# Kernel tuning notes

Hardware: AMD Instinct MI355X
Metric: run time of the kernel (lower is better)

The kernel has to match this reference:

```python
import jax, jax.numpy as jnp
import numpy as np

MEM_SIZE = 2000
FEA_DIM = 256
FMAP = 32
BATCH = 32
SHRINK = 0.0025
EPS = 1e-12


def setup_inputs() -> dict:
    key = jax.random.key(0)
    k1, k2, k3, k4 = jax.random.split(key, 4)
    stdv = 1.0 / np.sqrt(FEA_DIM)
    inp = {
        "input": jax.random.normal(k1, (BATCH, FEA_DIM, FMAP, FMAP), dtype=jnp.float32),
        "label_batch": jax.random.randint(k2, (BATCH,), 0, 2),
        "weight": jax.random.uniform(k3, (MEM_SIZE, FEA_DIM), dtype=jnp.float32, minval=-stdv, maxval=stdv),
        "pos_embedding": jax.random.normal(k4, (1, FEA_DIM, FMAP, FMAP), dtype=jnp.float32),
    }
    return inp


def _forward(x, weight, pos_embedding):
    b, c, h, w = x.shape
    m = weight.shape[0]
    x = x + pos_embedding  # pos=True
    xr = x.transpose(0, 2, 3, 1).reshape(-1, c)  # [b*h*w, c]
    # addressing: linear -> softmax over memory slots
    att = jax.nn.softmax(jnp.einsum('nc,mc->nm', xr, weight), axis=1)  # [N, m]
    # compact loss: MSE to nearest memory item (argmax of att before shrink)
    idx = jnp.argmax(att, axis=1)
    pos_item = weight[idx]  # [N, c]
    compact_loss = jnp.mean((xr - pos_item) ** 2)
    # distance loss: hinge on pairwise squared distances between memory items
    sq = jnp.sum(weight * weight, axis=1)
    d2 = sq[:, None] + sq[None, :] - 2.0 * (weight @ weight.T)  # [m, m]
    dist = 1.0 - d2
    dist = dist * (dist > 0).astype(dist.dtype)
    dist = jnp.triu(dist, k=1)
    distance_loss = dist.sum() * 2.0 / (m * (m - 1))
    # hard shrink relu + L1 normalize (shrink_thres > 0)
    att = jax.nn.relu(att - SHRINK) * att / (jnp.abs(att - SHRINK) + EPS)
    att = att / jnp.maximum(jnp.sum(jnp.abs(att), axis=1, keepdims=True), EPS)
    # memory read
    out = jnp.einsum('nm,mc->nc', att, weight)
    out = out.reshape(b, h, w, c).transpose(0, 3, 1, 2)
    return out, compact_loss, distance_loss


def reference(input, label_batch, weight, pos_embedding):
    return _forward(input, weight, pos_embedding)
```

## Files before the change

kernel.cpp:

```cpp
#include <hip/hip_runtime.h>
#include <hip/hip_bf16.h>

typedef unsigned char u8;
typedef unsigned short u16;
typedef unsigned int u32;
typedef long long s64;
typedef float f32x4 __attribute__((ext_vector_type(4)));
typedef long long s64x2 __attribute__((ext_vector_type(2)));

#define MEM    2000
#define FEA    256
#define SLSTR  2064
#define OSTR   265
#define XRS    264
#define POOLSZ 66048
#define OUTN   8388608

__device__ __forceinline__ u32 f2e4m3(float x) {
    float ax = fabsf(x);
    u32 s = (__builtin_bit_cast(u32, x) >> 24) & 0x80u;
    if (ax >= 448.f) return s | 0x7e;
    if (ax < 0.015625f) {
        int q = (int)rintf(ax * 512.f);
        return s | (u32)q;
    }
    int e = (int)(__builtin_bit_cast(u32, ax) >> 23) - 127;
    float scale = __builtin_bit_cast(float, (u32)((127 - e + 3) << 23));
    int q = (int)rintf(ax * scale);
    int E = e + 7;
    if (q == 16) { q = 8; E += 1; if (E > 15) return s | 0x7e; }
    return s | (u32)(E << 3) | (u32)(q & 7);
}
__device__ __forceinline__ u32 f2e4m3_fast(float v) {
    u32 u = __builtin_bit_cast(u32, v);
    u += 0x0007FFFFu + ((u >> 20) & 1u);
    int bb = (int)(u >> 20) - 0x3C0;
    return bb < 0 ? 0u : (u32)bb;
}

__global__ __launch_bounds__(256) void prep_kernel(const float* __restrict__ W,
                                                   u8* __restrict__ WTc,
                                                   u8* __restrict__ Wc,
                                                   float* __restrict__ sqv,
                                                   float* __restrict__ loss) {
    const int blk = blockIdx.x, t = threadIdx.x;
    const int m0 = blk * 8;
    {
        const int sl = t >> 5, cl = t & 31;
        const int slot = m0 + sl;
        const int ch0 = cl * 8;
        const float* wr = W + slot * 256 + ch0;
        f32x4 v0 = *(const f32x4*)wr;
        f32x4 v1 = *(const f32x4*)(wr + 4);
        float ss = v0[0]*v0[0] + v0[1]*v0[1] + v0[2]*v0[2] + v0[3]*v0[3]
                 + v1[0]*v1[0] + v1[1]*v1[1] + v1[2]*v1[2] + v1[3]*v1[3];
        ss += __shfl_xor(ss, 1); ss += __shfl_xor(ss, 2); ss += __shfl_xor(ss, 4);
        ss += __shfl_xor(ss, 8); ss += __shfl_xor(ss, 16);
        if (cl == 0) sqv[slot] = ss;
        const int c = slot >> 6, s = slot & 63;
        const int kk = cl >> 2, agp = cl & 3;
        const int kp = kk >> 1, klo = kk & 1;
        u32 lo = 0, hi = 0;
#pragma unroll
        for (int i = 0; i < 4; ++i) {
            lo |= f2e4m3(v0[i] * 16.f) << (i * 8);
            hi |= f2e4m3(v1[i] * 16.f) << (i * 8);
        }
        u8* dst = Wc + c * 16384 + (size_t)((kp * 4 + agp) * 64 + s) * 16 + klo * 8;
        *(u32*)dst = lo;
        *(u32*)(dst + 4) = hi;
    }
    {
        const int ch = t;
        const int chunk = m0 >> 6;
        const int kl0 = m0 & 63;
        const int klo = kl0 >> 5, agp = (kl0 & 31) >> 3;
        u32 lo = 0, hi = 0;
#pragma unroll
        for (int i = 0; i < 8; ++i) {
            u32 bb = f2e4m3(W[(m0 + i) * 256 + ch] * 16.f);
            if (i < 4) lo |= bb << (i * 8); else hi |= bb << ((i - 4) * 8);
        }
        u8* dst = WTc + chunk * 16384 + ch * 64 + agp * 16 + klo * 8;
        *(u32*)dst = lo;
        *(u32*)(dst + 4) = hi;
    }
    if (blk == 0 && t == 0) {
        loss[0] = 0.0f;
        loss[1] = -2000.0f / (2000.0f * 1999.0f);
    }
}

__global__ __launch_bounds__(512, 1) void main_kernel(
        const float* __restrict__ inp, const float* __restrict__ posb,
        const u8* __restrict__ Wc, const u8* __restrict__ WTc,
        const float* __restrict__ sqv, float* __restrict__ out,
        float* __restrict__ loss) {
    __shared__ __align__(16) u8 pool[POOLSZ];
    __shared__ float sPM[4][32];
    __shared__ int   sPI[4][32];
    __shared__ float sPZ[4][32];
    __shared__ float sPD[4][32];
    __shared__ float sSS[8][32];
    __shared__ float sMax[32];
    __shared__ float sThr[32];
    __shared__ float sInv[32];

    const int t = threadIdx.x;
    const int w = t >> 6, lane = t & 63;
    const int ar = lane & 15, ag = lane >> 4;
    const int blk = blockIdx.x, b = blk >> 5, hw0 = (blk & 31) << 5;
    const int prot = ((blk >> 3) & 15) * 2;
    const int q = w & 3, rt = w >> 2;
    const int row_a = rt * 16 + ar;

    {
        const int hw = t & 31, cg = t >> 5;
        const float* ip = inp + (size_t)b * 262144 + hw0 + hw;
        const float* pp = posb + hw0 + hw;
        float ss = 0.f;
        u8* xrow = pool + hw * XRS + cg * 16;
#pragma unroll
        for (int j = 0; j < 8; ++j) {
            const int ch = cg * 16 + 2 * j;
            float v0 = ip[ch * 1024] + pp[ch * 1024];
            float v1 = ip[(ch + 1) * 1024] + pp[(ch + 1) * 1024];
            ss += v0 * v0 + v1 * v1;
            u16 pk2 = (u16)(f2e4m3(v0 * 4.f) | (f2e4m3(v1 * 4.f) << 8));
            *(u16*)(xrow + 2 * j) = pk2;
        }
        ss += __shfl_xor(ss, 32);
        if (lane < 32) sSS[w][lane] = ss;
    }
    __syncthreads();

    s64 xB[8];
#pragma unroll
    for (int kk = 0; kk < 8; ++kk)
        xB[kk] = *(const s64*)(pool + row_a * XRS + kk * 32 + ag * 8);

    f32x4 acc[32];
    const int c31 = (31 - prot) & 31;
    {
        const u8* wbase = Wc + ag * 1024 + (q * 16 + ar) * 16;
#pragma unroll
        for (int c = 0; c < 32; ++c) {
            const int pc = (c + prot) & 31;
            const u8* p = wbase + pc * 16384;
            s64x2 w0 = *(const s64x2*)(p);
            s64x2 w1 = *(const s64x2*)(p + 4096);
            s64x2 w2 = *(const s64x2*)(p + 8192);
            s64x2 w3 = *(const s64x2*)(p + 12288);
            f32x4 a = {0.f, 0.f, 0.f, 0.f};
            a = __builtin_amdgcn_mfma_f32_16x16x32_fp8_fp8(w0[0], xB[0], a, 0, 0, 0);
            a = __builtin_amdgcn_mfma_f32_16x16x32_fp8_fp8(w0[1], xB[1], a, 0, 0, 0);
            a = __builtin_amdgcn_mfma_f32_16x16x32_fp8_fp8(w1[0], xB[2], a, 0, 0, 0);
            a = __builtin_amdgcn_mfma_f32_16x16x32_fp8_fp8(w1[1], xB[3], a, 0, 0, 0);
            a = __builtin_amdgcn_mfma_f32_16x16x32_fp8_fp8(w2[0], xB[4], a, 0, 0, 0);
            a = __builtin_amdgcn_mfma_f32_16x16x32_fp8_fp8(w2[1], xB[5], a, 0, 0, 0);
            a = __builtin_amdgcn_mfma_f32_16x16x32_fp8_fp8(w3[0], xB[6], a, 0, 0, 0);
            a = __builtin_amdgcn_mfma_f32_16x16x32_fp8_fp8(w3[1], xB[7], a, 0, 0, 0);
            if (c == c31 && q != 0) { a[0] = -3e38f; a[1] = -3e38f; a[2] = -3e38f; a[3] = -3e38f; }
            acc[c] = a;
        }
    }

    {
        float bm = -3e38f; int bi = 0x7fffffff;
#pragma unroll
        for (int c = 0; c < 32; ++c) {
            const int cb = (((c + prot) & 31) << 6) + q * 16 + ag * 4;
#pragma unroll
            for (int e = 0; e < 4; ++e) {
                float f = acc[c][e];
                int id = cb + e;
                if (f > bm || (f == bm && id < bi)) { bm = f; bi = id; }
            }
        }
#pragma unroll
        for (int d = 16; d < 64; d <<= 1) {
            float om = __shfl_xor(bm, d);
            int   oi = __shfl_xor(bi, d);
            if (om > bm || (om == bm && oi < bi)) { bm = om; bi = oi; }
        }
        if (lane < 16) { sPM[q][rt * 16 + lane] = bm; sPI[q][rt * 16 + lane] = bi; }
    }
    __syncthreads();

    if (t < 32) {
        float mx = sPM[0][t]; int bid = sPI[0][t];
#pragma unroll
        for (int qq = 1; qq < 4; ++qq) {
            float m2 = sPM[qq][t]; int i2 = sPI[qq][t];
            if (m2 > mx || (m2 == mx && i2 < bid)) { mx = m2; bid = i2; }
        }
        sMax[t] = mx;
        float ssq = 0.f;
#pragma unroll
        for (int ww = 0; ww < 8; ++ww) ssq += sSS[ww][t];
        float term = ssq - 2.f * (mx * 0.015625f) + sqv[bid];
#pragma unroll
        for (int d = 1; d < 32; d <<= 1) term += __shfl_xor(term, d);
        if (t == 0) atomicAdd(loss, term * (1.0f / 8388608.0f));
    }
    __syncthreads();

    {
        const float mxv = sMax[row_a];
        float z = 0.f;
#pragma unroll
        for (int c = 0; c < 32; ++c)
#pragma unroll
            for (int e = 0; e < 4; ++e) {
                float a_ = __expf((acc[c][e] - mxv) * 0.015625f);
                acc[c][e] = a_;
                z += a_;
            }
        z += __shfl_xor(z, 16); z += __shfl_xor(z, 32);
        if (lane < 16) sPZ[q][rt * 16 + lane] = z;
    }
    __syncthreads();
    if (t < 32) sThr[t] = 0.0025f * (sPZ[0][t] + sPZ[1][t] + sPZ[2][t] + sPZ[3][t]);
    __syncthreads();

    {
        const float thrv = sThr[row_a];
        const int newoff = (((q * 2 + (ag >> 1)) & 3) << 4) | ((q >> 1) << 3) | ((ag & 1) << 2);
        const int rowbase = row_a * SLSTR + newoff;
        float den = 0.f;
#pragma unroll
        for (int c = 0; c < 32; ++c) {
            const int off = rowbase + (((c + prot) & 31) << 6);
            u32 pk = 0;
#pragma unroll
            for (int e = 0; e < 4; ++e) {
                float a_ = acc[c][e];
                if (a_ > thrv) { den += a_; pk |= f2e4m3_fast(a_ * 64.f) << (e * 8); }
            }
            *(u32*)(pool + off) = pk;
        }
        den += __shfl_xor(den, 16); den += __shfl_xor(den, 32);
        if (lane < 16) sPD[q][rt * 16 + lane] = den;
    }
    __syncthreads();
    if (t < 32) {
        float dd = sPD[0][t] + sPD[1][t] + sPD[2][t] + sPD[3][t];
        sInv[t] = dd > 0.f ? 1.0f / (1024.0f * dd) : 0.0f;
    }
    __syncthreads();

    const int ch0 = (w * 2) * 16 + ar;
    const int ch1 = ch0 + 16;
    const u8* sLr0 = pool + ar * SLSTR + ag * 16;
    const u8* sLr1 = pool + (16 + ar) * SLSTR + ag * 16;
    const u8* wt0 = WTc + ch0 * 64 + ag * 16;
    const u8* wt1 = WTc + ch1 * 64 + ag * 16;
    f32x4 o00 = {0.f,0.f,0.f,0.f}, o01 = {0.f,0.f,0.f,0.f};
    f32x4 o10 = {0.f,0.f,0.f,0.f}, o11 = {0.f,0.f,0.f,0.f};
#pragma unroll
    for (int c = 0; c < 32; ++c) {
        const int pc = (c + prot) & 31;
        const int cc64 = pc << 6;
        s64x2 B0 = *(const s64x2*)(wt0 + pc * 16384);
        s64x2 B1 = *(const s64x2*)(wt1 + pc * 16384);
        s64x2 A0 = *(const s64x2*)(sLr0 + cc64);
        s64x2 A1 = *(const s64x2*)(sLr1 + cc64);
        o00 = __builtin_amdgcn_mfma_f32_16x16x32_fp8_fp8(A0[0], B0[0], o00, 0, 0, 0);
        o00 = __builtin_amdgcn_mfma_f32_16x16x32_fp8_fp8(A0[1], B0[1], o00, 0, 0, 0);
        o01 = __builtin_amdgcn_mfma_f32_16x16x32_fp8_fp8(A1[0], B0[0], o01, 0, 0, 0);
        o01 = __builtin_amdgcn_mfma_f32_16x16x32_fp8_fp8(A1[1], B0[1], o01, 0, 0, 0);
        o10 = __builtin_amdgcn_mfma_f32_16x16x32_fp8_fp8(A0[0], B1[0], o10, 0, 0, 0);
        o10 = __builtin_amdgcn_mfma_f32_16x16x32_fp8_fp8(A0[1], B1[1], o10, 0, 0, 0);
        o11 = __builtin_amdgcn_mfma_f32_16x16x32_fp8_fp8(A1[0], B1[0], o11, 0, 0, 0);
        o11 = __builtin_amdgcn_mfma_f32_16x16x32_fp8_fp8(A1[1], B1[1], o11, 0, 0, 0);
    }
    __syncthreads();

    {
        float* sO = (float*)pool;
#pragma unroll
        for (int i = 0; i < 4; ++i) {
            int r0 = ag * 4 + i, r1 = 16 + ag * 4 + i;
            sO[r0 * OSTR + ch0] = o00[i] * sInv[r0];
            sO[r1 * OSTR + ch0] = o01[i] * sInv[r1];
            sO[r0 * OSTR + ch1] = o10[i] * sInv[r0];
            sO[r1 * OSTR + ch1] = o11[i] * sInv[r1];
        }
    }
    __syncthreads();
    {
        const float* sO = (const float*)pool;
        const int hw = t & 31, cq = t >> 5;
        float* op = out + (size_t)b * 262144 + hw0 + hw;
#pragma unroll
        for (int i = 0; i < 16; ++i) {
            int ch = cq + (i << 4);
            op[ch * 1024] = sO[hw * OSTR + ch];
        }
    }
}

__global__ __launch_bounds__(256) void dist_kernel(const u8* __restrict__ Wc,
                                                   const float* __restrict__ sqv,
                                                   float* __restrict__ dl) {
    __shared__ float red[4];
    int t = threadIdx.x, w = t >> 6, lane = t & 63;
    int ar = lane & 15, ag = lane >> 4;
    const int i0 = blockIdx.x << 4;
    const int ci = i0 >> 6, si0 = i0 & 63;
    s64x2 af2[4];
#pragma unroll
    for (int kp = 0; kp < 4; ++kp)
        af2[kp] = *(const s64x2*)(Wc + ci * 16384 + (size_t)((kp * 4 + ag) * 64 + si0 + ar) * 16);
    float sqi[4];
#pragma unroll
    for (int e = 0; e < 4; ++e) sqi[e] = sqv[i0 + ag * 4 + e];
    float sum = 0.f;
    for (int jt = w; jt < 125; jt += 4) {
        const int j0 = jt << 4;
        const int cj = j0 >> 6, sj0 = j0 & 63;
        f32x4 acc = {0.f, 0.f, 0.f, 0.f};
#pragma unroll
        for (int kp = 0; kp < 4; ++kp) {
            s64x2 bf = *(const s64x2*)(Wc + cj * 16384 + (size_t)((kp * 4 + ag) * 64 + sj0 + ar) * 16);
            acc = __builtin_amdgcn_mfma_f32_16x16x32_fp8_fp8(af2[kp][0], bf[0], acc, 0, 0, 0);
            acc = __builtin_amdgcn_mfma_f32_16x16x32_fp8_fp8(af2[kp][1], bf[1], acc, 0, 0, 0);
        }
        float sqj = sqv[j0 + ar];
#pragma unroll
        for (int e = 0; e < 4; ++e) {
            float dist = 1.0f - (sqi[e] + sqj - acc[e] * 0.0078125f);
            sum += dist > 0.f ? dist : 0.f;
        }
    }
#pragma unroll
    for (int d = 1; d < 64; d <<= 1) sum += __shfl_xor(sum, d);
    if (lane == 0) red[w] = sum;
    __syncthreads();
    if (t == 0) {
        float s = red[0] + red[1] + red[2] + red[3];
        atomicAdd(dl, s * (1.0f / (2000.0f * 1999.0f)));
    }
}

extern "C" void kernel_launch(void* const* d_in, const int* in_sizes, int n_in,
                              void* d_out, int out_size, void* d_ws, size_t ws_size,
                              hipStream_t stream) {
    (void)in_sizes; (void)n_in; (void)out_size; (void)ws_size;
    const float* inp  = (const float*)d_in[0];
    const float* W    = (const float*)d_in[2];
    const float* posb = (const float*)d_in[3];
    float* out = (float*)d_out;

    u8* WTc = (u8*)d_ws;
    u8* Wc  = (u8*)d_ws + 524288;
    float* sqv = (float*)((u8*)d_ws + 1048576);

    hipLaunchKernelGGL(prep_kernel, dim3(250), dim3(256), 0, stream, W, WTc, Wc, sqv, out + OUTN);
    hipLaunchKernelGGL(main_kernel, dim3(1024), dim3(512), 0, stream, inp, posb, Wc, WTc, sqv, out, out + OUTN);
    hipLaunchKernelGGL(dist_kernel, dim3(125), dim3(256), 0, stream, Wc, sqv, out + OUTN + 1);
}
```

Before: 169.2 us.

## Recompute logits with online softmax instead of holding 128 accumulators in registers

Instead of keeping all 32 f32x4 logit tiles live in registers, the kernel computes an online (streaming) max/argmax and rescaled softmax sum in the first MFMA pass. It then recomputes the logits in a second MFMA pass to apply the threshold and pack to fp8. This drops one reduction phase and two barriers, and cuts register pressure enough to raise launch bounds from 1 to 4 blocks per CU. The cost is doubling the fp8 MFMA work and the weight reads from global/L2, plus extra exp calls for the online rescaling.

```diff
diff --git a/kernel.cpp b/kernel.cpp
--- a/kernel.cpp
+++ b/kernel.cpp
@@ -15,6 +15,7 @@
 #define XRS    264
 #define POOLSZ 66048
 #define OUTN   8388608
+#define LSC    0.015625f
 
 __device__ __forceinline__ u32 f2e4m3(float x) {
     float ax = fabsf(x);
@@ -91,7 +92,7 @@
     }
 }
 
-__global__ __launch_bounds__(512, 1) void main_kernel(
+__global__ __launch_bounds__(512, 4) void main_kernel(
         const float* __restrict__ inp, const float* __restrict__ posb,
         const u8* __restrict__ Wc, const u8* __restrict__ WTc,
         const float* __restrict__ sqv, float* __restrict__ out,
@@ -139,10 +140,12 @@
     for (int kk = 0; kk < 8; ++kk)
         xB[kk] = *(const s64*)(pool + row_a * XRS + kk * 32 + ag * 8);
 
-    f32x4 acc[32];
+    const u8* wbase = Wc + ag * 1024 + (q * 16 + ar) * 16;
     const int c31 = (31 - prot) & 31;
-    {
-        const u8* wbase = Wc + ag * 1024 + (q * 16 + ar) * 16;
+
+    {
+        float bm = -3e38f, zz = 0.f;
+        int bi = 0x7fffffff;
 #pragma unroll
         for (int c = 0; c < 32; ++c) {
             const int pc = (c + prot) & 31;
@@ -161,44 +164,55 @@
             a = __builtin_amdgcn_mfma_f32_16x16x32_fp8_fp8(w3[0], xB[6], a, 0, 0, 0);
             a = __builtin_amdgcn_mfma_f32_16x16x32_fp8_fp8(w3[1], xB[7], a, 0, 0, 0);
             if (c == c31 && q != 0) { a[0] = -3e38f; a[1] = -3e38f; a[2] = -3e38f; a[3] = -3e38f; }
-            acc[c] = a;
-        }
-    }
-
-    {
-        float bm = -3e38f; int bi = 0x7fffffff;
-#pragma unroll
-        for (int c = 0; c < 32; ++c) {
-            const int cb = (((c + prot) & 31) << 6) + q * 16 + ag * 4;
+            const int cb = (pc << 6) + q * 16 + ag * 4;
+            const float ob = bm;
 #pragma unroll
             for (int e = 0; e < 4; ++e) {
-                float f = acc[c][e];
-                int id = cb + e;
-                if (f > bm || (f == bm && id < bi)) { bm = f; bi = id; }
+                float v = a[e]; int id = cb + e;
+                bool g = (v > bm) || (v == bm && id < bi);
+                bm = g ? v : bm;
+                bi = g ? id : bi;
             }
+            zz *= __expf((ob - bm) * LSC);
+            zz += __expf((a[0] - bm) * LSC) + __expf((a[1] - bm) * LSC)
+                + __expf((a[2] - bm) * LSC) + __expf((a[3] - bm) * LSC);
         }
 #pragma unroll
         for (int d = 16; d < 64; d <<= 1) {
             float om = __shfl_xor(bm, d);
             int   oi = __shfl_xor(bi, d);
-            if (om > bm || (om == bm && oi < bi)) { bm = om; bi = oi; }
-        }
-        if (lane < 16) { sPM[q][rt * 16 + lane] = bm; sPI[q][rt * 16 + lane] = bi; }
+            float oz = __shfl_xor(zz, d);
+            bool g = (om > bm) || (om == bm && oi < bi);
+            float nm = g ? om : bm;
+            zz = zz * __expf((bm - nm) * LSC) + oz * __expf((om - nm) * LSC);
+            bm = nm;
+            bi = g ? oi : bi;
+        }
+        if (lane < 16) {
+            sPM[q][rt * 16 + lane] = bm;
+            sPI[q][rt * 16 + lane] = bi;
+            sPZ[q][rt * 16 + lane] = zz;
+        }
     }
     __syncthreads();
 
     if (t < 32) {
-        float mx = sPM[0][t]; int bid = sPI[0][t];
+        float M = sPM[0][t]; int I = sPI[0][t];
 #pragma unroll
         for (int qq = 1; qq < 4; ++qq) {
             float m2 = sPM[qq][t]; int i2 = sPI[qq][t];
-            if (m2 > mx || (m2 == mx && i2 < bid)) { mx = m2; bid = i2; }
-        }
-        sMax[t] = mx;
+            bool g = (m2 > M) || (m2 == M && i2 < I);
+            M = g ? m2 : M; I = g ? i2 : I;
+        }
+        float Z = 0.f;
+#pragma unroll
+        for (int qq = 0; qq < 4; ++qq) Z += sPZ[qq][t] * __expf((sPM[qq][t] - M) * LSC);
+        sMax[t] = M;
+        sThr[t] = 0.0025f * Z;
         float ssq = 0.f;
 #pragma unroll
         for (int ww = 0; ww < 8; ++ww) ssq += sSS[ww][t];
-        float term = ssq - 2.f * (mx * 0.015625f) + sqv[bid];
+        float term = ssq - 2.f * (M * LSC) + sqv[I];
 #pragma unroll
         for (int d = 1; d < 32; d <<= 1) term += __shfl_xor(term, d);
         if (t == 0) atomicAdd(loss, term * (1.0f / 8388608.0f));
@@ -206,40 +220,43 @@
     __syncthreads();
 
     {
-        const float mxv = sMax[row_a];
-        float z = 0.f;
-#pragma unroll
-        for (int c = 0; c < 32; ++c)
-#pragma unroll
-            for (int e = 0; e < 4; ++e) {
-                float a_ = __expf((acc[c][e] - mxv) * 0.015625f);
-                acc[c][e] = a_;
-                z += a_;
-            }
-        z += __shfl_xor(z, 16); z += __shfl_xor(z, 32);
-        if (lane < 16) sPZ[q][rt * 16 + lane] = z;
-    }
-    __syncthreads();
-    if (t < 32) sThr[t] = 0.0025f * (sPZ[0][t] + sPZ[1][t] + sPZ[2][t] + sPZ[3][t]);
-    __syncthreads();
-
-    {
+        const float M = sMax[row_a];
         const float thrv = sThr[row_a];
         const int newoff = (((q * 2 + (ag >> 1)) & 3) << 4) | ((q >> 1) << 3) | ((ag & 1) << 2);
         const int rowbase = row_a * SLSTR + newoff;
         float den = 0.f;
 #pragma unroll
         for (int c = 0; c < 32; ++c) {
-            const int off = rowbase + (((c + prot) & 31) << 6);
-            u32 pk = 0;
-#pragma unroll
-            for (int e = 0; e < 4; ++e) {
-                float a_ = acc[c][e];
-                if (a_ > thrv) { den += a_; pk |= f2e4m3_fast(a_ * 64.f) << (e * 8); }
-            }
-            *(u32*)(pool + off) = pk;
-        }
-        den += __shfl_xor(den, 16); den += __shfl_xor(den, 32);
+            const int pc = (c + prot) & 31;
+            const u8* p = wbase + pc * 16384;
+            s64x2 w0 = *(const s64x2*)(p);
+            s64x2 w1 = *(const s64x2*)(p + 4096);
+            s64x2 w2 = *(const s64x2*)(p + 8192);
+            s64x2 w3 = *(const s64x2*)(p + 12288);
+            f32x4 a = {0.f, 0.f, 0.f, 0.f};
+            a = __builtin_amdgcn_mfma_f32_16x16x32_fp8_fp8(w0[0], xB[0], a, 0, 0, 0);
+            a = __builtin_amdgcn_mfma_f32_16x16x32_fp8_fp8(w0[1], xB[1], a, 0, 0, 0);
+            a = __builtin_amdgcn_mfma_f32_16x16x32_fp8_fp8(w1[0], xB[2], a, 0, 0, 0);
+            a = __builtin_amdgcn_mfma_f32_16x16x32_fp8_fp8(w1[1], xB[3], a, 0, 0, 0);
+            a = __builtin_amdgcn_mfma_f32_16x16x32_fp8_fp8(w2[0], xB[4], a, 0, 0, 0);
+            a = __builtin_amdgcn_mfma_f32_16x16x32_fp8_fp8(w2[1], xB[5], a, 0, 0, 0);
+            a = __builtin_amdgcn_mfma_f32_16x16x32_fp8_fp8(w3[0], xB[6], a, 0, 0, 0);
+            a = __builtin_amdgcn_mfma_f32_16x16x32_fp8_fp8(w3[1], xB[7], a, 0, 0, 0);
+            if (c == c31 && q != 0) { a[0] = -3e38f; a[1] = -3e38f; a[2] = -3e38f; a[3] = -3e38f; }
+            float a0 = __expf((a[0] - M) * LSC);
+            float a1 = __expf((a[1] - M) * LSC);
+            float a2 = __expf((a[2] - M) * LSC);
+            float a3 = __expf((a[3] - M) * LSC);
+            bool k0 = a0 > thrv, k1 = a1 > thrv, k2 = a2 > thrv, k3 = a3 > thrv;
+            den += (k0 ? a0 : 0.f) + (k1 ? a1 : 0.f) + (k2 ? a2 : 0.f) + (k3 ? a3 : 0.f);
+            u32 pk = (k0 ? f2e4m3_fast(a0 * 64.f) : 0u)
+                   | ((k1 ? f2e4m3_fast(a1 * 64.f) : 0u) << 8)
+                   | ((k2 ? f2e4m3_fast(a2 * 64.f) : 0u) << 16)
+                   | ((k3 ? f2e4m3_fast(a3 * 64.f) : 0u) << 24);
+            *(u32*)(pool + rowbase + (pc << 6)) = pk;
+        }
+        den += __shfl_xor(den, 16);
+        den += __shfl_xor(den, 32);
         if (lane < 16) sPD[q][rt * 16 + lane] = den;
     }
     __syncthreads();
```

Result: slower. 383.5 us (+126.7%).
